# Kernel tuning notes

Measured on AMD Instinct MI355X. Metric: run time of the kernel, lower is better.

The kernel has to match this reference:

```python
import jax, jax.numpy as jnp
import numpy as np

B, N, N2 = 4, 2048, 1024
DIM, DIM_Y, H = 1024, 1024, 16
HD = DIM // H  # head_dim = 64
SCALE = HD ** -0.5


def setup_inputs() -> dict:
    key = jax.random.key(0)
    ks = jax.random.split(key, 6)
    s = 0.02
    return {
        "x": jax.random.normal(ks[0], (B, N, DIM), dtype=jnp.float32),
        "y": jax.random.normal(ks[1], (B, N2, DIM_Y), dtype=jnp.float32),
        "pad_mask": jax.random.randint(ks[2], (B, N2), 0, 2, dtype=jnp.int32),
        "Wq": jax.random.normal(ks[3], (DIM, DIM), dtype=jnp.float32) * s,
        "Wkv": jax.random.normal(ks[4], (DIM_Y, 2 * DIM), dtype=jnp.float32) * s,
        "Wproj": jax.random.normal(ks[5], (DIM, DIM), dtype=jnp.float32) * s,
        "bproj": jnp.zeros((DIM,), dtype=jnp.float32),
    }


def reference(x, y, pad_mask, Wq, Wkv, Wproj, bproj):
    b, n, c = x.shape
    n2 = y.shape[1]
    # projections (no bias on q/kv, per qkv_bias=False)
    q = (x @ Wq).reshape(b, n, H, HD).transpose(0, 2, 1, 3)          # [B,H,N,HD]
    kv = (y @ Wkv).reshape(b, n2, 2, H, HD).transpose(2, 0, 3, 1, 4)  # [2,B,H,N2,HD]
    k, v = kv[0], kv[1]
    # scaled attention scores with key-side pad mask
    scores = jnp.einsum("bhnd,bhmd->bhnm", q * SCALE, k)             # [B,H,N,N2]
    keep = pad_mask.astype(bool)[:, None, None, :]                   # [B,1,1,N2]
    scores = jnp.where(keep, scores, -jnp.inf)
    attn = jax.nn.softmax(scores, axis=-1)
    out = jnp.einsum("bhnm,bhmd->bhnd", attn, v)                     # [B,H,N,HD]
    out = out.transpose(0, 2, 1, 3).reshape(b, n, c)
    return out @ Wproj + bproj
```

## Files before the change

### kernel.cpp

```cpp
#include <hip/hip_runtime.h>

typedef unsigned short u16;
typedef unsigned int   u32;
typedef unsigned long long u64;
using bf16x8 = __bf16 __attribute__((ext_vector_type(8)));
using f32x4  = float  __attribute__((ext_vector_type(4)));
using f32x16 = float  __attribute__((ext_vector_type(16)));
using u32x2  = u32    __attribute__((ext_vector_type(2)));

#define B_    4
#define N_    2048
#define N2_   1024
#define DIM_  1024
#define H_    16
#define HD_   64
#define SCALE_ 0.125f
#define LOG2E_ 1.4426950408889634f

union PU { u32 w[4]; bf16x8 v; };

__device__ __forceinline__ u16 f2bf(float f) {
  unsigned u = __float_as_uint(f);
  u += 0x7fffu + ((u >> 16) & 1u);
  return (u16)(u >> 16);
}

__device__ __forceinline__ u32 packbf(float lo, float hi) {
  union { __bf16 b[2]; u32 u; } c;
  c.b[0] = (__bf16)lo; c.b[1] = (__bf16)hi;
  return c.u;
}

__device__ __forceinline__ float pair_sum(float x) { return x + __shfl_xor(x, 32); }

__device__ __forceinline__ void gload16(const u16* g, u16* l) {
  __builtin_amdgcn_global_load_lds(
      (const __attribute__((address_space(1))) u32*)g,
      (__attribute__((address_space(3))) u32*)l, 16, 0, 0);
}

__global__ __launch_bounds__(256) void scan_mask(
    const int* __restrict__ pad, int* __restrict__ kidx, int* __restrict__ Nkeep)
{
  const int w = threadIdx.x >> 6, lane = threadIdx.x & 63;
  int base = 0;
#pragma unroll
  for (int c = 0; c < 16; ++c) {
    const int idx = c*64 + lane;
    const int keep = pad[w*N2_ + idx] != 0;
    const u64 m = __ballot(keep);
    const int pre = __popcll(m & ((1ull << lane) - 1ull));
    if (keep) kidx[w*N2_ + base + pre] = idx;
    base += __popcll(m);
  }
  for (int j = base + lane; j < N2_; j += 64) kidx[w*N2_ + j] = 0;
  if (lane == 0) Nkeep[w] = base;
}

__global__ __launch_bounds__(256) void cvt_fused(
    const float* __restrict__ x, const float* __restrict__ y,
    const int* __restrict__ kidx, const int* __restrict__ Nkeep,
    u16* __restrict__ xb, u16* __restrict__ yc)
{
  const int id = blockIdx.x * 256 + threadIdx.x;
  union { u32 w[4]; uint4 u; } c;
  if (id < 1048576) {
    const int i = id * 8;
    const float4 a = *(const float4*)&x[i];
    const float4 b = *(const float4*)&x[i + 4];
    c.w[0] = packbf(a.x, a.y); c.w[1] = packbf(a.z, a.w);
    c.w[2] = packbf(b.x, b.y); c.w[3] = packbf(b.z, b.w);
    *(uint4*)&xb[i] = c.u;
  } else {
    const int e8 = (id - 1048576) * 8;
    const int b   = e8 >> 20;
    const int j   = (e8 >> 10) & 1023;
    const int col = e8 & 1023;
    if (j < Nkeep[b]) {
      const int row = kidx[b*N2_ + j];
      const float* src = &y[((size_t)(b*N2_ + row))*DIM_ + col];
      const float4 a0 = *(const float4*)&src[0];
      const float4 a1 = *(const float4*)&src[4];
      c.w[0] = packbf(a0.x, a0.y); c.w[1] = packbf(a0.z, a0.w);
      c.w[2] = packbf(a1.x, a1.y); c.w[3] = packbf(a1.z, a1.w);
    } else {
      c.w[0] = c.w[1] = c.w[2] = c.w[3] = 0u;
    }
    *(uint4*)&yc[(size_t)(b*N2_ + j)*DIM_ + col] = c.u;
  }
}

__global__ __launch_bounds__(256) void transpose_w_all(
    const float* __restrict__ Wq, const float* __restrict__ Wkv,
    const float* __restrict__ Wproj,
    u16* __restrict__ WqT, u16* __restrict__ WkvT, u16* __restrict__ WprojT)
{
  const int z = blockIdx.z;
  const float* W; u16* Wt; int Nc;
  if      (z == 0) { W = Wq;    Wt = WqT;    Nc = 1024; }
  else if (z == 1) { W = Wkv;   Wt = WkvT;   Nc = 2048; }
  else             { W = Wproj; Wt = WprojT; Nc = 1024; }
  const int n0 = blockIdx.x * 32, k0 = blockIdx.y * 32;
  if (n0 >= Nc) return;
  __shared__ float t[32][33];
  const int tx = threadIdx.x, ty = threadIdx.y;
#pragma unroll
  for (int i = 0; i < 4; ++i)
    t[ty + 8*i][tx] = W[(size_t)(k0 + ty + 8*i) * Nc + n0 + tx];
  __syncthreads();
#pragma unroll
  for (int i = 0; i < 4; ++i)
    Wt[(size_t)(n0 + ty + 8*i) * 1024 + k0 + tx] = f2bf(t[tx][ty + 8*i]);
}

#define GEMM_SHARED                                                            \
  __shared__ __align__(16) u16 As[2][128 * 64];                                \
  __shared__ __align__(16) u16 Bs[2][128 * 64];

#define STAGE(buf, k0) {                                                       \
    _Pragma("unroll")                                                          \
    for (int i = 0; i < 4; ++i) {                                              \
      gload16(ga + (size_t)(8*i)*1024 + (k0), &As[buf][(wave*4 + i) * 512]);   \
      gload16(gb + (size_t)(8*i)*1024 + (k0), &Bs[buf][(wave*4 + i) * 512]);   \
    } }

#define GEMM_BODY(A, Bt, CW)                                                   \
  const int tid = threadIdx.x;                                                 \
  const int lane = tid & 63, wave = tid >> 6;                                  \
  const int wr = wave >> 1, wc = wave & 1;                                     \
  const int lr = lane & 15, lg = lane >> 4;                                    \
  f32x4 acc[4][4] = {};                                                        \
  const int l8 = lane >> 3;                                                    \
  const int c8 = ((lane & 7) ^ l8) * 8;                                        \
  const u16* ga = &A [(size_t)(m0 + 32*wave + l8) * 1024 + c8];                \
  const u16* gb = &Bt[(size_t)(n0 + 32*wave + l8) * 1024 + c8];                \
  STAGE(0, 0);                                                                 \
  __syncthreads();                                                             \
  int cur = 0;                                                                 \
  for (int t = 0; t < 16; ++t) {                                               \
    if (t + 1 < 16) STAGE(cur ^ 1, (t + 1) * 64);                              \
    _Pragma("unroll")                                                          \
    for (int kk = 0; kk < 2; ++kk) {                                           \
      bf16x8 af[4], bfr[4];                                                    \
      _Pragma("unroll")                                                        \
      for (int m = 0; m < 4; ++m) {                                            \
        const int row = wr*64 + m*16 + lr;                                     \
        af[m] = *(const bf16x8*)&As[cur][row*64 + (((kk*4 + lg) ^ (row & 7)) * 8)]; \
      }                                                                        \
      _Pragma("unroll")                                                        \
      for (int n = 0; n < 4; ++n) {                                            \
        const int row = wc*64 + n*16 + lr;                                     \
        bfr[n] = *(const bf16x8*)&Bs[cur][row*64 + (((kk*4 + lg) ^ (row & 7)) * 8)]; \
      }                                                                        \
      __builtin_amdgcn_s_setprio(1);                                           \
      _Pragma("unroll")                                                        \
      for (int m = 0; m < 4; ++m)                                              \
        _Pragma("unroll")                                                      \
        for (int n = 0; n < 4; ++n)                                            \
          acc[m][n] = __builtin_amdgcn_mfma_f32_16x16x32_bf16(af[m], bfr[n], acc[m][n], 0, 0, 0); \
      __builtin_amdgcn_s_setprio(0);                                           \
    }                                                                          \
    __syncthreads();                                                           \
    cur ^= 1;                                                                  \
  }                                                                            \
  _Pragma("unroll")                                                            \
  for (int m = 0; m < 4; ++m)                                                  \
    _Pragma("unroll")                                                          \
    for (int n = 0; n < 4; ++n)                                                \
      _Pragma("unroll")                                                        \
      for (int j = 0; j < 4; ++j) {                                            \
        const int r = m0 + wr*64 + m*16 + lg*4 + j;                            \
        const int c = n0 + wc*64 + n*16 + lr;                                  \
        CW;                                                                    \
      }

__global__ __launch_bounds__(256) void gemm3(
    const u16* __restrict__ xb, const u16* __restrict__ yc,
    const u16* __restrict__ WqT, const u16* __restrict__ WkvT,
    const int* __restrict__ Nkeep,
    u16* __restrict__ Qb, u16* __restrict__ Kc, u16* __restrict__ Cvt)
{
  GEMM_SHARED
  const int bx = blockIdx.x;
  if (bx < 512) {
    const int xcd = bx & 7, slot = bx >> 3;
    const int m0 = (xcd*8 + (slot & 7)) * 128;
    const int n0 = (slot >> 3) * 128;
    GEMM_BODY(xb, WqT,
      Qb[(size_t)r * 1024 + c] = f2bf(acc[m][n][j] * (SCALE_*LOG2E_)));
  } else if (bx < 768) {
    const int i = bx - 512;
    const int xcd = i & 7, slot = i >> 3;
    const int m0 = (xcd*4 + (slot & 3)) * 128;
    const int n0 = (slot >> 2) * 128;
    if ((m0 & 1023) >= Nkeep[m0 >> 10]) return;
    GEMM_BODY(yc, WkvT,
      Kc[(size_t)r * 1024 + c] = f2bf(acc[m][n][j]));
  } else {
    const int i = bx - 768;
    const int xcd = i & 7, slot = i >> 3;
    const int m0 = (slot >> 2) * 128;
    const int n0 = (xcd*4 + (slot & 3)) * 128;
    if ((n0 & 1023) >= Nkeep[n0 >> 10]) return;
    const u16* Wv = WkvT + (size_t)1024 * 1024;
    GEMM_BODY(Wv, yc,
      Cvt[(size_t)r * 4096 + c] = f2bf(acc[m][n][j]));
  }
}

__global__ __launch_bounds__(256) void gemm_proj(
    const u16* __restrict__ A, const u16* __restrict__ Bt,
    const float* __restrict__ bias, float* __restrict__ C)
{
  GEMM_SHARED
  const int m0 = blockIdx.y * 128, n0 = blockIdx.x * 128;
  GEMM_BODY(A, Bt,
    C[(size_t)r * 1024 + c] = acc[m][n][j] + bias[c]);
}

#define QKSTEP(S, QF) { \
    const int c_ = (((S)*2 + hi) ^ x7) * 8; \
    const bf16x8 ka_ = *(const bf16x8*)&Ks[lq*64 + c_]; \
    const bf16x8 kb_ = *(const bf16x8*)&Ks[(32+lq)*64 + c_]; \
    s0 = __builtin_amdgcn_mfma_f32_32x32x16_bf16(ka_, QF, s0, 0, 0, 0); \
    s1 = __builtin_amdgcn_mfma_f32_32x32x16_bf16(kb_, QF, s1, 0, 0, 0); }

__global__ __launch_bounds__(512) void attn2(
    const u16* __restrict__ Q, const u16* __restrict__ Kc,
    const u16* __restrict__ Cvt, const int* __restrict__ Nkeep,
    u16* __restrict__ AO)
{
  const int bh = blockIdx.x, qt = blockIdx.y;
  const int b = bh >> 4, h = bh & 15;
  const int tid = threadIdx.x;
  const int wave = tid >> 6, lane = tid & 63;
  const int lq = lane & 31, hi = lane >> 5;
  const int x7 = lq & 7;

  __shared__ __align__(16) u16 Ks[64*64];
  __shared__ __align__(16) u16 Vs[64*64];
  __shared__ __align__(16) u32 Ps[8][32][36];

  const int nk  = Nkeep[b];
  const int nkr = (nk + 63) & ~63;

  const int qrow = qt*256 + wave*32 + lq;
  const size_t qbase = ((size_t)b*N_ + qrow)*DIM_ + h*HD_;
  const bf16x8 qf0 = *(const bf16x8*)&Q[qbase +  0 + hi*8];
  const bf16x8 qf1 = *(const bf16x8*)&Q[qbase + 16 + hi*8];
  const bf16x8 qf2 = *(const bf16x8*)&Q[qbase + 32 + hi*8];
  const bf16x8 qf3 = *(const bf16x8*)&Q[qbase + 48 + hi*8];

  f32x16 o0 = {}, o1 = {}, sacc = {};

  const int srow = tid >> 3, schk = tid & 7;
  const int swz = (schk ^ (srow & 7)) * 8;
  const u16* kp = &Kc[(size_t)b*N2_*1024 + h*HD_ + (size_t)srow*1024 + schk*8];
  const u16* vp = &Cvt[(size_t)(h*HD_ + srow)*4096 + b*N2_ + schk*8];
  u32 (*pw)[36] = Ps[wave];

  uint4 kw = *(const uint4*)kp;
  uint4 vw = *(const uint4*)vp;

  for (int kt = 0; kt < nkr; kt += 64) {
    f32x16 s0 = {}, s1 = {};
    if (kt + 64 > nk) {
#pragma unroll
      for (int r = 0; r < 16; ++r) {
        const int key = kt + (r & 3) + 8*(r >> 2) + 4*hi;
        if (key      >= nk) s0[r] = -30000.f;
        if (key + 32 >= nk) s1[r] = -30000.f;
      }
    }

    __syncthreads();
    *(uint4*)&Ks[srow*64 + swz] = kw;
    *(uint4*)&Vs[srow*64 + swz] = vw;
    __syncthreads();

    if (kt + 64 < nkr) {
      kw = *(const uint4*)(kp + (size_t)(kt + 64)*1024);
      vw = *(const uint4*)(vp + (kt + 64));
    }

    __builtin_amdgcn_s_setprio(1);
    QKSTEP(0, qf0); QKSTEP(1, qf1); QKSTEP(2, qf2); QKSTEP(3, qf3);
    __builtin_amdgcn_s_setprio(0);

#pragma unroll
    for (int r = 0; r < 16; ++r) {
      s0[r] = exp2f(s0[r]);
      s1[r] = exp2f(s1[r]);
      sacc[r] += s0[r] + s1[r];
    }

#pragma unroll
    for (int g = 0; g < 4; ++g) {
      u32x2 wa, wb;
      wa[0] = packbf(s0[4*g+0], s0[4*g+1]);
      wa[1] = packbf(s0[4*g+2], s0[4*g+3]);
      wb[0] = packbf(s1[4*g+0], s1[4*g+1]);
      wb[1] = packbf(s1[4*g+2], s1[4*g+3]);
      *(u32x2*)&pw[lq][     4*g + 2*hi] = wa;
      *(u32x2*)&pw[lq][16 + 4*g + 2*hi] = wb;
    }
    asm volatile("" ::: "memory");

    __builtin_amdgcn_s_setprio(1);
#pragma unroll
    for (int KS = 0; KS < 4; ++KS) {
      PU pu;
#pragma unroll
      for (int j = 0; j < 4; ++j) pu.w[j] = pw[lq][KS*8 + 4*hi + j];
      const int c_ = ((KS*2 + hi) ^ x7) * 8;
      const bf16x8 va = *(const bf16x8*)&Vs[lq*64 + c_];
      const bf16x8 vb = *(const bf16x8*)&Vs[(32+lq)*64 + c_];
      o0 = __builtin_amdgcn_mfma_f32_32x32x16_bf16(va, pu.v, o0, 0, 0, 0);
      o1 = __builtin_amdgcn_mfma_f32_32x32x16_bf16(vb, pu.v, o1, 0, 0, 0);
    }
    __builtin_amdgcn_s_setprio(0);
  }

#pragma unroll
  for (int d = 8; d >= 1; d >>= 1)
#pragma unroll
    for (int r = 0; r < 8; ++r) if (r < d) sacc[r] += sacc[r + d];
  const float lsum = pair_sum(sacc[0]);

  const float rls = 1.f / lsum;
  const size_t obase = ((size_t)b*N_ + qrow)*DIM_ + h*HD_;
#pragma unroll
  for (int g = 0; g < 4; ++g) {
    u32x2 w;
    w[0] = packbf(o0[4*g+0]*rls, o0[4*g+1]*rls);
    w[1] = packbf(o0[4*g+2]*rls, o0[4*g+3]*rls);
    *(u32x2*)&AO[obase + 8*g + 4*hi] = w;
    w[0] = packbf(o1[4*g+0]*rls, o1[4*g+1]*rls);
    w[1] = packbf(o1[4*g+2]*rls, o1[4*g+3]*rls);
    *(u32x2*)&AO[obase + 32 + 8*g + 4*hi] = w;
  }
}

extern "C" void kernel_launch(void* const* d_in, const int* in_sizes, int n_in,
                              void* d_out, int out_size, void* d_ws, size_t ws_size,
                              hipStream_t stream)
{
  const float* x     = (const float*)d_in[0];
  const float* y     = (const float*)d_in[1];
  const int*   pad   = (const int*)  d_in[2];
  const float* Wq    = (const float*)d_in[3];
  const float* Wkv   = (const float*)d_in[4];
  const float* Wproj = (const float*)d_in[5];
  const float* bproj = (const float*)d_in[6];

  char* ws = (char*)d_ws;
  u16* Kc     = (u16*)(ws);
  u16* Cvt    = (u16*)(ws + (size_t)( 8<<20));
  u16* yc     = (u16*)(ws + (size_t)(16<<20));
  u16* WqT    = (u16*)(ws + (size_t)(24<<20));
  u16* WkvT   = (u16*)(ws + (size_t)(26<<20));
  u16* WprojT = (u16*)(ws + (size_t)(30<<20));
  u16* Qb     = (u16*)(ws + (size_t)(32<<20));
  u16* AOb    = (u16*)(ws + (size_t)(48<<20));
  u16* xb     = (u16*)d_out;
  int* kidx   = (int*)((char*)d_out + (size_t)(16<<20));
  int* Nkeep  = kidx + B_*N2_;

  const dim3 tb(32, 8);
  scan_mask<<<dim3(1), 256, 0, stream>>>(pad, kidx, Nkeep);
  cvt_fused<<<dim3(6144), 256, 0, stream>>>(x, y, kidx, Nkeep, xb, yc);
  transpose_w_all<<<dim3(64, 32, 3), tb, 0, stream>>>(Wq, Wkv, Wproj,
                                                      WqT, WkvT, WprojT);
  gemm3<<<dim3(1024), 256, 0, stream>>>(xb, yc, WqT, WkvT, Nkeep,
                                        Qb, Kc, Cvt);
  attn2<<<dim3(64, 8), 512, 0, stream>>>(Qb, Kc, Cvt, Nkeep, AOb);
  gemm_proj<<<dim3(8, 64), 256, 0, stream>>>(AOb, WprojT, bproj,
                                             (float*)d_out);
}
```

Before: 137.0 us.

## Stage K/V in 128-key chunks in attention and XCD-swizzle proj GEMM tiles

The attention kernel now loads K and V into shared memory two 64-key tiles at a time, with prefetch registers covering 128 keys, so block-wide barriers happen once per 128 keys instead of twice per 64. Shared memory for K/V doubles and register pressure rises from the extra prefetch registers. The projection GEMM moves to a 1D grid with an XCD-aware tile mapping, so each XCD works on a contiguous band of rows for better L2 locality.

```diff
diff --git a/kernel.cpp b/kernel.cpp
--- a/kernel.cpp
+++ b/kernel.cpp
@@ -213,15 +213,18 @@
     const float* __restrict__ bias, float* __restrict__ C)
 {
   GEMM_SHARED
-  const int m0 = blockIdx.y * 128, n0 = blockIdx.x * 128;
+  const int bx = blockIdx.x;
+  const int xcd = bx & 7, slot = bx >> 3;
+  const int m0 = (xcd*8 + (slot & 7)) * 128;
+  const int n0 = (slot >> 3) * 128;
   GEMM_BODY(A, Bt,
     C[(size_t)r * 1024 + c] = acc[m][n][j] + bias[c]);
 }
 
 #define QKSTEP(S, QF) { \
     const int c_ = (((S)*2 + hi) ^ x7) * 8; \
-    const bf16x8 ka_ = *(const bf16x8*)&Ks[lq*64 + c_]; \
-    const bf16x8 kb_ = *(const bf16x8*)&Ks[(32+lq)*64 + c_]; \
+    const bf16x8 ka_ = *(const bf16x8*)&Ks[(hbase + lq)*64 + c_]; \
+    const bf16x8 kb_ = *(const bf16x8*)&Ks[(hbase + 32 + lq)*64 + c_]; \
     s0 = __builtin_amdgcn_mfma_f32_32x32x16_bf16(ka_, QF, s0, 0, 0, 0); \
     s1 = __builtin_amdgcn_mfma_f32_32x32x16_bf16(kb_, QF, s1, 0, 0, 0); }
 
@@ -237,8 +240,8 @@
   const int lq = lane & 31, hi = lane >> 5;
   const int x7 = lq & 7;
 
-  __shared__ __align__(16) u16 Ks[64*64];
-  __shared__ __align__(16) u16 Vs[64*64];
+  __shared__ __align__(16) u16 Ks[128*64];
+  __shared__ __align__(16) u16 Vs[64*128];
   __shared__ __align__(16) u32 Ps[8][32][36];
 
   const int nk  = Nkeep[b];
@@ -259,10 +262,32 @@
   const u16* vp = &Cvt[(size_t)(h*HD_ + srow)*4096 + b*N2_ + schk*8];
   u32 (*pw)[36] = Ps[wave];
 
-  uint4 kw = *(const uint4*)kp;
-  uint4 vw = *(const uint4*)vp;
+  uint4 kw0, kw1, vw0, vw1;
+#define LREG(kt) { \
+    kw0 = *(const uint4*)(kp + (size_t)(kt)*1024); \
+    kw1 = *(const uint4*)(kp + (size_t)((kt)+64)*1024); \
+    vw0 = *(const uint4*)(vp + (kt)); \
+    vw1 = *(const uint4*)(vp + (kt) + 64); }
+#define WBUF() { \
+    *(uint4*)&Ks[srow*64 + swz] = kw0; \
+    *(uint4*)&Ks[(srow+64)*64 + swz] = kw1; \
+    *(uint4*)&Vs[srow*128 + swz] = vw0; \
+    *(uint4*)&Vs[srow*128 + 64 + swz] = vw1; }
+
+  LREG(0);
+  WBUF();
+  if (nkr > 128) LREG(128);
+  __syncthreads();
 
   for (int kt = 0; kt < nkr; kt += 64) {
+    if ((kt & 127) == 0 && kt > 0) {
+      __syncthreads();
+      WBUF();
+      __syncthreads();
+      if (kt + 128 < nkr) LREG(kt + 128);
+    }
+    const int hbase = kt & 64;
+
     f32x16 s0 = {}, s1 = {};
     if (kt + 64 > nk) {
 #pragma unroll
@@ -271,16 +296,6 @@
         if (key      >= nk) s0[r] = -30000.f;
         if (key + 32 >= nk) s1[r] = -30000.f;
       }
-    }
-
-    __syncthreads();
-    *(uint4*)&Ks[srow*64 + swz] = kw;
-    *(uint4*)&Vs[srow*64 + swz] = vw;
-    __syncthreads();
-
-    if (kt + 64 < nkr) {
-      kw = *(const uint4*)(kp + (size_t)(kt + 64)*1024);
-      vw = *(const uint4*)(vp + (kt + 64));
     }
 
     __builtin_amdgcn_s_setprio(1);
@@ -312,14 +327,16 @@
       PU pu;
 #pragma unroll
       for (int j = 0; j < 4; ++j) pu.w[j] = pw[lq][KS*8 + 4*hi + j];
-      const int c_ = ((KS*2 + hi) ^ x7) * 8;
-      const bf16x8 va = *(const bf16x8*)&Vs[lq*64 + c_];
-      const bf16x8 vb = *(const bf16x8*)&Vs[(32+lq)*64 + c_];
+      const int c_ = hbase + ((KS*2 + hi) ^ x7) * 8;
+      const bf16x8 va = *(const bf16x8*)&Vs[lq*128 + c_];
+      const bf16x8 vb = *(const bf16x8*)&Vs[(32+lq)*128 + c_];
       o0 = __builtin_amdgcn_mfma_f32_32x32x16_bf16(va, pu.v, o0, 0, 0, 0);
       o1 = __builtin_amdgcn_mfma_f32_32x32x16_bf16(vb, pu.v, o1, 0, 0, 0);
     }
     __builtin_amdgcn_s_setprio(0);
   }
+#undef LREG
+#undef WBUF
 
 #pragma unroll
   for (int d = 8; d >= 1; d >>= 1)
@@ -374,6 +391,6 @@
   gemm3<<<dim3(1024), 256, 0, stream>>>(xb, yc, WqT, WkvT, Nkeep,
                                         Qb, Kc, Cvt);
   attn2<<<dim3(64, 8), 512, 0, stream>>>(Qb, Kc, Cvt, Nkeep, AOb);
-  gemm_proj<<<dim3(8, 64), 256, 0, stream>>>(AOb, WprojT, bproj,
-                                             (float*)d_out);
-}
+  gemm_proj<<<dim3(512), 256, 0, stream>>>(AOb, WprojT, bproj,
+                                           (float*)d_out);
+}
```

New measurement: 136.7 us. No clear change (-0.2%).

## Double-buffer attention K/V via direct-to-LDS loads, single-buffer GEMMs, remap proj grid

Applied to the files above, without the earlier changes.

The attention kernel now stages K and V tiles with direct global-to-LDS loads into two LDS buffers, prefetching the next tile while computing the current one. This replaces the register round-trip with two barriers per iteration. The row-sum is reduced per tile into a scalar instead of a 16-wide accumulator, which lowers register pressure. The shared GEMM body drops its double buffer in favour of a load-sync-compute-sync loop, which halves LDS use but exposes load latency. gemm_proj switches to a 1D grid with an XCD-aware block mapping.

```diff
diff --git a/kernel.cpp b/kernel.cpp
--- a/kernel.cpp
+++ b/kernel.cpp
@@ -114,14 +114,14 @@
 }
 
 #define GEMM_SHARED                                                            \
-  __shared__ __align__(16) u16 As[2][128 * 64];                                \
-  __shared__ __align__(16) u16 Bs[2][128 * 64];
-
-#define STAGE(buf, k0) {                                                       \
+  __shared__ __align__(16) u16 As[128 * 64];                                   \
+  __shared__ __align__(16) u16 Bs[128 * 64];
+
+#define STAGE(k0) {                                                            \
     _Pragma("unroll")                                                          \
     for (int i = 0; i < 4; ++i) {                                              \
-      gload16(ga + (size_t)(8*i)*1024 + (k0), &As[buf][(wave*4 + i) * 512]);   \
-      gload16(gb + (size_t)(8*i)*1024 + (k0), &Bs[buf][(wave*4 + i) * 512]);   \
+      gload16(ga + (size_t)(8*i)*1024 + (k0), &As[(wave*4 + i) * 512]);        \
+      gload16(gb + (size_t)(8*i)*1024 + (k0), &Bs[(wave*4 + i) * 512]);        \
     } }
 
 #define GEMM_BODY(A, Bt, CW)                                                   \
@@ -134,23 +134,21 @@
   const int c8 = ((lane & 7) ^ l8) * 8;                                        \
   const u16* ga = &A [(size_t)(m0 + 32*wave + l8) * 1024 + c8];                \
   const u16* gb = &Bt[(size_t)(n0 + 32*wave + l8) * 1024 + c8];                \
-  STAGE(0, 0);                                                                 \
-  __syncthreads();                                                             \
-  int cur = 0;                                                                 \
   for (int t = 0; t < 16; ++t) {                                               \
-    if (t + 1 < 16) STAGE(cur ^ 1, (t + 1) * 64);                              \
+    STAGE(t * 64);                                                             \
+    __syncthreads();                  \
     _Pragma("unroll")                                                          \
     for (int kk = 0; kk < 2; ++kk) {                                           \
       bf16x8 af[4], bfr[4];                                                    \
       _Pragma("unroll")                                                        \
       for (int m = 0; m < 4; ++m) {                                            \
         const int row = wr*64 + m*16 + lr;                                     \
-        af[m] = *(const bf16x8*)&As[cur][row*64 + (((kk*4 + lg) ^ (row & 7)) * 8)]; \
+        af[m] = *(const bf16x8*)&As[row*64 + (((kk*4 + lg) ^ (row & 7)) * 8)]; \
       }                                                                        \
       _Pragma("unroll")                                                        \
       for (int n = 0; n < 4; ++n) {                                            \
         const int row = wc*64 + n*16 + lr;                                     \
-        bfr[n] = *(const bf16x8*)&Bs[cur][row*64 + (((kk*4 + lg) ^ (row & 7)) * 8)]; \
+        bfr[n] = *(const bf16x8*)&Bs[row*64 + (((kk*4 + lg) ^ (row & 7)) * 8)]; \
       }                                                                        \
       __builtin_amdgcn_s_setprio(1);                                           \
       _Pragma("unroll")                                                        \
@@ -160,8 +158,7 @@
           acc[m][n] = __builtin_amdgcn_mfma_f32_16x16x32_bf16(af[m], bfr[n], acc[m][n], 0, 0, 0); \
       __builtin_amdgcn_s_setprio(0);                                           \
     }                                                                          \
-    __syncthreads();                                                           \
-    cur ^= 1;                                                                  \
+    __syncthreads();         \
   }                                                                            \
   _Pragma("unroll")                                                            \
   for (int m = 0; m < 4; ++m)                                                  \
@@ -213,15 +210,18 @@
     const float* __restrict__ bias, float* __restrict__ C)
 {
   GEMM_SHARED
-  const int m0 = blockIdx.y * 128, n0 = blockIdx.x * 128;
+  const int bx = blockIdx.x;
+  const int xcd = bx & 7, slot = bx >> 3;
+  const int m0 = (xcd*8 + (slot & 7)) * 128;
+  const int n0 = (slot >> 3) * 128;
   GEMM_BODY(A, Bt,
     C[(size_t)r * 1024 + c] = acc[m][n][j] + bias[c]);
 }
 
-#define QKSTEP(S, QF) { \
+#define QKSTEP(S, QF, KB) { \
     const int c_ = (((S)*2 + hi) ^ x7) * 8; \
-    const bf16x8 ka_ = *(const bf16x8*)&Ks[lq*64 + c_]; \
-    const bf16x8 kb_ = *(const bf16x8*)&Ks[(32+lq)*64 + c_]; \
+    const bf16x8 ka_ = *(const bf16x8*)&KB[lq*64 + c_]; \
+    const bf16x8 kb_ = *(const bf16x8*)&KB[(32+lq)*64 + c_]; \
     s0 = __builtin_amdgcn_mfma_f32_32x32x16_bf16(ka_, QF, s0, 0, 0, 0); \
     s1 = __builtin_amdgcn_mfma_f32_32x32x16_bf16(kb_, QF, s1, 0, 0, 0); }
 
@@ -237,8 +237,8 @@
   const int lq = lane & 31, hi = lane >> 5;
   const int x7 = lq & 7;
 
-  __shared__ __align__(16) u16 Ks[64*64];
-  __shared__ __align__(16) u16 Vs[64*64];
+  __shared__ __align__(16) u16 Ks[2][64*64];
+  __shared__ __align__(16) u16 Vs[2][64*64];
   __shared__ __align__(16) u32 Ps[8][32][36];
 
   const int nk  = Nkeep[b];
@@ -251,18 +251,26 @@
   const bf16x8 qf2 = *(const bf16x8*)&Q[qbase + 32 + hi*8];
   const bf16x8 qf3 = *(const bf16x8*)&Q[qbase + 48 + hi*8];
 
-  f32x16 o0 = {}, o1 = {}, sacc = {};
-
-  const int srow = tid >> 3, schk = tid & 7;
-  const int swz = (schk ^ (srow & 7)) * 8;
-  const u16* kp = &Kc[(size_t)b*N2_*1024 + h*HD_ + (size_t)srow*1024 + schk*8];
-  const u16* vp = &Cvt[(size_t)(h*HD_ + srow)*4096 + b*N2_ + schk*8];
+  f32x16 o0 = {}, o1 = {};
+  float sacc1 = 0.f;
+
+  const int l8 = lane >> 3;
+  const int c8 = ((lane & 7) ^ l8) * 8;
+  const u16* gk = &Kc[(size_t)b*N2_*1024 + h*HD_ + (size_t)(8*wave + l8)*1024 + c8];
+  const u16* gv = &Cvt[(size_t)(h*HD_ + 8*wave + l8)*4096 + b*N2_ + c8];
   u32 (*pw)[36] = Ps[wave];
 
-  uint4 kw = *(const uint4*)kp;
-  uint4 vw = *(const uint4*)vp;
-
+#define GSTAGE(buf, kt) { \
+    gload16(gk + (size_t)(kt)*1024, &Ks[buf][wave*512]); \
+    gload16(gv + (kt),              &Vs[buf][wave*512]); }
+
+  GSTAGE(0, 0);
+  __syncthreads();
+
+  int cur = 0;
   for (int kt = 0; kt < nkr; kt += 64) {
+    if (kt + 64 < nkr) GSTAGE(cur ^ 1, kt + 64);
+
     f32x16 s0 = {}, s1 = {};
     if (kt + 64 > nk) {
 #pragma unroll
@@ -273,25 +281,25 @@
       }
     }
 
-    __syncthreads();
-    *(uint4*)&Ks[srow*64 + swz] = kw;
-    *(uint4*)&Vs[srow*64 + swz] = vw;
-    __syncthreads();
-
-    if (kt + 64 < nkr) {
-      kw = *(const uint4*)(kp + (size_t)(kt + 64)*1024);
-      vw = *(const uint4*)(vp + (kt + 64));
-    }
-
     __builtin_amdgcn_s_setprio(1);
-    QKSTEP(0, qf0); QKSTEP(1, qf1); QKSTEP(2, qf2); QKSTEP(3, qf3);
+    QKSTEP(0, qf0, Ks[cur]); QKSTEP(1, qf1, Ks[cur]);
+    QKSTEP(2, qf2, Ks[cur]); QKSTEP(3, qf3, Ks[cur]);
     __builtin_amdgcn_s_setprio(0);
 
 #pragma unroll
     for (int r = 0; r < 16; ++r) {
       s0[r] = exp2f(s0[r]);
       s1[r] = exp2f(s1[r]);
-      sacc[r] += s0[r] + s1[r];
+    }
+    {
+      f32x16 sm;
+#pragma unroll
+      for (int r = 0; r < 16; ++r) sm[r] = s0[r] + s1[r];
+#pragma unroll
+      for (int d = 8; d >= 1; d >>= 1)
+#pragma unroll
+        for (int r = 0; r < 8; ++r) if (r < d) sm[r] += sm[r + d];
+      sacc1 += sm[0];
     }
 
 #pragma unroll
@@ -313,20 +321,19 @@
 #pragma unroll
       for (int j = 0; j < 4; ++j) pu.w[j] = pw[lq][KS*8 + 4*hi + j];
       const int c_ = ((KS*2 + hi) ^ x7) * 8;
-      const bf16x8 va = *(const bf16x8*)&Vs[lq*64 + c_];
-      const bf16x8 vb = *(const bf16x8*)&Vs[(32+lq)*64 + c_];
+      const bf16x8 va = *(const bf16x8*)&Vs[cur][lq*64 + c_];
+      const bf16x8 vb = *(const bf16x8*)&Vs[cur][(32+lq)*64 + c_];
       o0 = __builtin_amdgcn_mfma_f32_32x32x16_bf16(va, pu.v, o0, 0, 0, 0);
       o1 = __builtin_amdgcn_mfma_f32_32x32x16_bf16(vb, pu.v, o1, 0, 0, 0);
     }
     __builtin_amdgcn_s_setprio(0);
-  }
-
-#pragma unroll
-  for (int d = 8; d >= 1; d >>= 1)
-#pragma unroll
-    for (int r = 0; r < 8; ++r) if (r < d) sacc[r] += sacc[r + d];
-  const float lsum = pair_sum(sacc[0]);
-
+
+    __syncthreads();
+    cur ^= 1;
+  }
+#undef GSTAGE
+
+  const float lsum = pair_sum(sacc1);
   const float rls = 1.f / lsum;
   const size_t obase = ((size_t)b*N_ + qrow)*DIM_ + h*HD_;
 #pragma unroll
@@ -374,6 +381,6 @@
   gemm3<<<dim3(1024), 256, 0, stream>>>(xb, yc, WqT, WkvT, Nkeep,
                                         Qb, Kc, Cvt);
   attn2<<<dim3(64, 8), 512, 0, stream>>>(Qb, Kc, Cvt, Nkeep, AOb);
-  gemm_proj<<<dim3(8, 64), 256, 0, stream>>>(AOb, WprojT, bproj,
-                                             (float*)d_out);
-}
+  gemm_proj<<<dim3(512), 256, 0, stream>>>(AOb, WprojT, bproj,
+                                           (float*)d_out);
+}
```

New measurement: 133.8 us. 2.3% less time.
